# Kernel tuning notes

Measured on AMD Instinct MI355X. Metric: run time of the kernel, lower is better.

Reference implementation:

```python
import jax, jax.numpy as jnp
import numpy as np

H = 12          # nheads
SIM_EPS = 1e-8  # SimMatrix eps
LN_EPS = 1e-5   # nn.LayerNorm default eps
SLOPE = 0.01    # LeakyReLU default negative slope


def leaky(x):
    return jnp.where(x >= 0, x, SLOPE * x)


def etc_attention(hiddens, gamma, beta, Wout, bout):
    # hiddens: [B, L, 3*D]
    B, L, D3 = hiddens.shape
    D = D3 // 3
    d = D // H
    h = hiddens.reshape(B, L, 3, H, d)
    Q = h[:, :, 0].transpose(0, 2, 1, 3)  # [B,H,L,d]
    K = h[:, :, 1].transpose(0, 2, 1, 3)
    V = h[:, :, 2].transpose(0, 2, 1, 3)
    # cosine-similarity attention scores (SimMatrix(K, Q))
    Kn = K / jnp.clip(jnp.linalg.norm(K, axis=-1, keepdims=True), SIM_EPS, None)
    Qn = Q / jnp.clip(jnp.linalg.norm(Q, axis=-1, keepdims=True), SIM_EPS, None)
    att = jnp.einsum('bhid,bhjd->bhij', Kn, Qn)  # [B,H,L,L]
    # LayerNorm over the head axis H (lnormalize: [B, L*L, H] layernorm on last dim)
    mu = att.mean(axis=1, keepdims=True)
    var = att.var(axis=1, keepdims=True)  # biased, matches torch LayerNorm
    att = (att - mu) / jnp.sqrt(var + LN_EPS)
    att = att * gamma[None, :, None, None] + beta[None, :, None, None]
    att = jax.nn.softmax(att, axis=-1)
    att = jnp.where(jnp.isnan(att), jnp.zeros_like(att), att)  # removeNaN
    out = jnp.einsum('bhij,bhjd->bhid', att, V)          # att @ V
    out = out.transpose(0, 2, 1, 3).reshape(B, L, D)      # catHiddens
    # dropout is identity at inference; lin_out = Linear + Softmax
    probs = jax.nn.softmax(out @ Wout.T + bout, axis=-1)  # [B,L,C]
    return probs, att


def get_weights(att, masks):
    # att: [B,H,L,L], masks: [B,L] float
    w = masks * att.mean(axis=1).sum(axis=1)  # [B,L]
    return jax.nn.softmax(w, axis=-1)[..., None]  # [B,L,1]


def setup_inputs() -> dict:
    key = jax.random.key(0)
    ks = jax.random.split(key, 16)
    B, L = 16, 512
    Din, D, C, VOCAB = 300, 768, 20, 32000

    def kaiming(k, shape, fan_in):
        return jax.random.normal(k, shape, jnp.float32) * np.sqrt(2.0 / fan_in)

    return {
        'input_ids': jax.random.randint(ks[0], (B, L), 0, VOCAB),
        'wv': jax.random.normal(ks[1], (B, L, Din), jnp.float32),
        'emb': jax.random.normal(ks[2], (VOCAB, D), jnp.float32),
        'W_t': kaiming(ks[3], (3 * D, D), D),
        'b_t': jnp.zeros((3 * D,), jnp.float32),
        'gamma_t': jnp.ones((H,), jnp.float32),
        'beta_t': jnp.zeros((H,), jnp.float32),
        'Wout_t': kaiming(ks[4], (C, D), D),
        'bout_t': jnp.zeros((C,), jnp.float32),
        'W_h': kaiming(ks[5], (3 * D, Din), Din),
        'b_h': jnp.zeros((3 * D,), jnp.float32),
        'gamma_h': jnp.ones((H,), jnp.float32),
        'beta_h': jnp.zeros((H,), jnp.float32),
        'Wout_h': kaiming(ks[6], (C, D), D),
        'bout_h': jnp.zeros((C,), jnp.float32),
    }


def reference(input_ids, wv, emb, W_t, b_t, gamma_t, beta_t, Wout_t, bout_t,
              W_h, b_h, gamma_h, beta_h, Wout_h, bout_h):
    masks = (input_ids != 0).astype(jnp.float32)  # [B,L]
    # token branch: Embedding -> LeakyReLU -> Linear -> LeakyReLU
    h_t = leaky(leaky(emb[input_ids]) @ W_t.T + b_t)
    probs_t, att_t = etc_attention(h_t, gamma_t, beta_t, Wout_t, bout_t)
    probs_t = (get_weights(att_t, masks) * probs_t).sum(axis=1)  # [B,C]
    # hidden/word-vector branch: Linear -> LeakyReLU
    h_h = leaky(wv @ W_h.T + b_h)
    probs_h, att_h = etc_attention(h_h, gamma_h, beta_h, Wout_h, bout_h)
    probs_h = (get_weights(att_h, masks) * probs_h).sum(axis=1)
    return (probs_t + probs_h) / 2.0
```

## Files before the change

kernel.cpp:

```cpp
#include <hip/hip_runtime.h>

typedef unsigned int uint;
typedef unsigned short ushort;
typedef _Float16 f16;
typedef _Float16 h8 __attribute__((ext_vector_type(8)));
typedef float f32x4 __attribute__((ext_vector_type(4)));


__device__ __forceinline__ float b2f(ushort u){ return __uint_as_float(((uint)u)<<16); }
__device__ __forceinline__ ushort f2b(float f){
  uint u = __float_as_uint(f);
  uint r = u + 0x7fffu + ((u>>16)&1u);
  return (ushort)(r>>16);
}
__device__ __forceinline__ float leaky(float x){ return x >= 0.f ? x : 0.01f*x; }
__device__ __forceinline__ float ldf(const void* p, int idx, int isb){
  return isb ? b2f(((const ushort*)p)[idx]) : ((const float*)p)[idx];
}

#define GLOAD16(gp, lp) __builtin_amdgcn_global_load_lds( \
    (const __attribute__((address_space(1))) void*)(gp), \
    (__attribute__((address_space(3))) void*)(lp), 16, 0, 0)

__global__ __launch_bounds__(256) void k_init(const ushort* __restrict__ wvbits,
    int* __restrict__ flag, float* __restrict__ zbase){
  int bid = blockIdx.x, tid = threadIdx.x;
  if (bid == 0){
    if (tid == 0){
      int sane = 0;
      for (int i=0;i<128;i++){
        uint e = (wvbits[i]>>7)&0xffu;
        if (e==0u || (e>=90u && e<=150u)) sane++;
      }
      *flag = (sane >= 115) ? 1 : 0;
    }
  } else {
    zbase[(bid-1)*256 + tid] = 0.f;
  }
}

__global__ __launch_bounds__(256) void k_prep_all(const int* __restrict__ ids,
    const void* __restrict__ emb, const void* __restrict__ wv,
    const void* __restrict__ W0, const void* __restrict__ W1,
    const int* __restrict__ flag,
    f16* __restrict__ AhA, f16* __restrict__ WhA,
    f16* __restrict__ AhB, f16* __restrict__ WhB,
    int nBX, int nW0, int nA1, int nW1){
  int isb = *flag;
  int bx = blockIdx.x, tid = threadIdx.x;
  if (bx < nBX){
    int t = bx*256 + tid;
    int m = t / 96, kk = (t % 96) * 8;
    float o[8];
    if (isb){
      const ushort* src = (const ushort*)emb + (size_t)ids[m]*768 + kk;
      uint4 v = *(const uint4*)src;
      o[0]=__uint_as_float((v.x&0xffffu)<<16); o[1]=__uint_as_float(v.x&0xffff0000u);
      o[2]=__uint_as_float((v.y&0xffffu)<<16); o[3]=__uint_as_float(v.y&0xffff0000u);
      o[4]=__uint_as_float((v.z&0xffffu)<<16); o[5]=__uint_as_float(v.z&0xffff0000u);
      o[6]=__uint_as_float((v.w&0xffffu)<<16); o[7]=__uint_as_float(v.w&0xffff0000u);
    } else {
      const float* src = (const float*)emb + (size_t)ids[m]*768 + kk;
      float4 v0 = ((const float4*)src)[0];
      float4 v1 = ((const float4*)src)[1];
      o[0]=v0.x; o[1]=v0.y; o[2]=v0.z; o[3]=v0.w;
      o[4]=v1.x; o[5]=v1.y; o[6]=v1.z; o[7]=v1.w;
    }
    h8 hv;
    #pragma unroll
    for (int i=0;i<8;i++) hv[i] = (f16)leaky(o[i]);
    *(h8*)(AhA + (size_t)m*768 + kk) = hv;
  } else if (bx < nBX + nW0){
    int t = (bx - nBX)*256 + tid;
    int n = t / 96, kk = (t % 96) * 8;
    h8 hv;
    #pragma unroll
    for (int i=0;i<8;i++) hv[i] = (f16)ldf(W0, n*768 + kk + i, isb);
    *(h8*)(WhA + (size_t)n*768 + kk) = hv;
  } else if (bx < nBX + nW0 + nA1){
    int t = (bx - nBX - nW0)*256 + tid;
    int n = t / 40, kk = (t % 40) * 8;
    h8 hv;
    #pragma unroll
    for (int i=0;i<8;i++){
      int k = kk + i;
      hv[i] = (k < 300) ? (f16)ldf(wv, n*300 + k, isb) : (f16)0.f;
    }
    *(h8*)(AhB + (size_t)n*320 + kk) = hv;
  } else {
    int t = (bx - nBX - nW0 - nA1)*256 + tid;
    int n = t / 40, kk = (t % 40) * 8;
    h8 hv;
    #pragma unroll
    for (int i=0;i<8;i++){
      int k = kk + i;
      hv[i] = (k < 300) ? (f16)ldf(W1, n*300 + k, isb) : (f16)0.f;
    }
    *(h8*)(WhB + (size_t)n*320 + kk) = hv;
  }
}

__global__ __launch_bounds__(256) void k_gemm_m(
    const f16* AhA, const f16* WhA, const void* biasA, int KA,
    f16* QhA, f16* KhA, f16* VtA,
    const f16* AhB, const f16* WhB, const void* biasB, int KB,
    f16* QhB, f16* KhB, f16* VtB,
    const int* __restrict__ flag, int sbase){
  __shared__ __align__(16) f16 As[128*64];
  __shared__ __align__(16) f16 Bs[128*64];
  int z = sbase + blockIdx.z;
  const f16* Ah = z ? AhB : AhA;
  const f16* Wh = z ? WhB : WhA;
  const void* bias = z ? biasB : biasA;
  int KP = z ? KB : KA;
  f16* Qh = z ? QhB : QhA;
  f16* Kh = z ? KhB : KhA;
  f16* Vt = z ? VtB : VtA;
  int STEPS = KP >> 6;

  int tid = threadIdx.x;
  int w = tid >> 6, lane = tid & 63;
  int mrow = lane & 15, kq = lane >> 4;
  int m0 = (((blockIdx.x & 7)<<3) | (blockIdx.x >> 3)) * 128;
  int n0 = blockIdx.y * 128;
  int msub = (w & 1) * 64, nsub = (w >> 1) * 64;

  f32x4 acc[4][4];
  #pragma unroll
  for (int mt=0; mt<4; mt++)
    #pragma unroll
    for (int nt=0; nt<4; nt++) acc[mt][nt] = (f32x4){0.f,0.f,0.f,0.f};

  int cbase = w*64 + lane;

  for (int step=0; step<STEPS; step++){
    int k0 = step*64;
    __syncthreads();
    #pragma unroll
    for (int rep=0; rep<4; rep++){
      int cb = rep*256 + w*64;
      int c  = rep*256 + cbase;
      int row = c >> 3;
      int qs  = (c & 7) ^ (row & 7);
      GLOAD16(Ah + (size_t)(m0+row)*KP + k0 + qs*8, As + cb*8);
      GLOAD16(Wh + (size_t)(n0+row)*KP + k0 + qs*8, Bs + cb*8);
    }
    __syncthreads();
    #pragma unroll
    for (int ks=0; ks<2; ks++){
      h8 af[4], bf[4];
      #pragma unroll
      for (int mt=0; mt<4; mt++){
        int row = msub + mt*16 + mrow;
        int slot = (ks*4 + kq) ^ (row & 7);
        af[mt] = *(const h8*)(As + row*64 + slot*8);
      }
      #pragma unroll
      for (int nt=0; nt<4; nt++){
        int row = nsub + nt*16 + mrow;
        int slot = (ks*4 + kq) ^ (row & 7);
        bf[nt] = *(const h8*)(Bs + row*64 + slot*8);
      }
      #pragma unroll
      for (int mt=0; mt<4; mt++)
        #pragma unroll
        for (int nt=0; nt<4; nt++)
          acc[mt][nt] = __builtin_amdgcn_mfma_f32_16x16x32_f16(af[mt], bf[nt], acc[mt][nt], 0, 0, 0);
    }
  }

  int isb = *flag;
  int n0w = n0 + nsub;
  int s = n0w / 768;
  int h = (n0w % 768) >> 6;
  float bv[4];
  #pragma unroll
  for (int nt=0; nt<4; nt++) bv[nt] = ldf(bias, n0w + nt*16 + mrow, isb);

  #pragma unroll
  for (int mt=0; mt<4; mt++){
    float yv[4][4];
    #pragma unroll
    for (int nt=0; nt<4; nt++)
      #pragma unroll
      for (int r=0; r<4; r++)
        yv[nt][r] = leaky(acc[mt][nt][r] + bv[nt]);
    if (s < 2){
      #pragma unroll
      for (int r=0; r<4; r++){
        float ss = yv[0][r]*yv[0][r] + yv[1][r]*yv[1][r]
                 + yv[2][r]*yv[2][r] + yv[3][r]*yv[3][r];
        ss += __shfl_xor(ss, 1); ss += __shfl_xor(ss, 2);
        ss += __shfl_xor(ss, 4); ss += __shfl_xor(ss, 8);
        float rn = 1.f / fmaxf(sqrtf(ss), 1e-8f);
        #pragma unroll
        for (int nt=0; nt<4; nt++) yv[nt][r] *= rn;
      }
    }
    #pragma unroll
    for (int nt=0; nt<4; nt++){
      #pragma unroll
      for (int r=0; r<4; r++){
        int m = m0 + msub + mt*16 + kq*4 + r;
        int dd = nt*16 + mrow;
        int bq = m >> 9, l = m & 511;
        float y = yv[nt][r];
        if (s == 0)      Qh[((size_t)(bq*12 + h)*512 + l)*64 + dd] = (f16)y;
        else if (s == 1) Kh[((size_t)(bq*12 + h)*512 + l)*64 + dd] = (f16)y;
        else             Vt[((size_t)(bq*12 + h)*64 + dd)*512 + l] = (f16)y;
      }
    }
  }
}

__global__ __launch_bounds__(256) void k_scores(const f16* __restrict__ Qh,
    const f16* __restrict__ Kh, const void* __restrict__ gamma,
    const void* __restrict__ beta, const int* __restrict__ flag,
    f16* __restrict__ E, float* __restrict__ lsump){
  constexpr int TS = 72;
  __shared__ f16 S[12*16*TS];
  __shared__ float gL[12], beL[12];

  int tid = threadIdx.x;
  int w = tid >> 6, lane = tid & 63;
  int kq = lane >> 4, mrow = lane & 15;
  int bx = (blockIdx.x & 7)*512 + (blockIdx.x >> 3);
  int jt = bx & 7, it = (bx >> 3) & 31, b = bx >> 8;
  int i0 = it*16, j0 = jt*64;

  if (tid < 12){ int isb = *flag; gL[tid] = ldf(gamma, tid, isb); beL[tid] = ldf(beta, tid, isb); }

  #pragma unroll
  for (int hh=0; hh<3; hh++){
    int h = w*3 + hh;
    const f16* kb = Kh + ((size_t)(b*12+h)*512 + i0 + mrow)*64;
    h8 a0 = *(const h8*)(kb + kq*8);
    h8 a1 = *(const h8*)(kb + 32 + kq*8);
    const f16* qb = Qh + ((size_t)(b*12+h)*512 + j0)*64;
    #pragma unroll
    for (int jn=0; jn<4; jn++){
      const f16* qr = qb + (size_t)(jn*16 + mrow)*64;
      h8 q0 = *(const h8*)(qr + kq*8);
      h8 q1 = *(const h8*)(qr + 32 + kq*8);
      f32x4 c = (f32x4){0.f,0.f,0.f,0.f};
      c = __builtin_amdgcn_mfma_f32_16x16x32_f16(a0, q0, c, 0, 0, 0);
      c = __builtin_amdgcn_mfma_f32_16x16x32_f16(a1, q1, c, 0, 0, 0);
      #pragma unroll
      for (int r=0;r<4;r++)
        S[(h*16 + kq*4 + r)*TS + jn*16 + mrow] = (f16)c[r];
    }
  }
  __syncthreads();
  int pj = tid & 63, piw = tid >> 6;
  #pragma unroll
  for (int p=0; p<4; p++){
    int i = piw*4 + p;
    float s[12];
    float mu = 0.f, sq = 0.f;
    #pragma unroll
    for (int h=0;h<12;h++){ s[h] = (float)S[(h*16+i)*TS + pj]; mu += s[h]; sq += s[h]*s[h]; }
    mu *= (1.f/12.f);
    float var = fmaxf(sq*(1.f/12.f) - mu*mu, 0.f);
    float rstd = rsqrtf(var + 1e-5f);
    #pragma unroll
    for (int h=0;h<12;h++){
      float e = __expf((s[h]-mu)*rstd*gL[h] + beL[h]);
      S[(h*16+i)*TS + pj] = (f16)e;
    }
  }
  __syncthreads();
  if (tid < 192){
    int h = tid >> 4, i = tid & 15;
    const f16* zr = &S[(h*16 + i)*TS];
    float ssum = 0.f;
    #pragma unroll
    for (int q=0;q<8;q++){
      h8 v = *(const h8*)(zr + q*8);
      #pragma unroll
      for (int t=0;t<8;t++) ssum += (float)v[t];
    }
    lsump[((size_t)(b*12+h)*512 + i0 + i)*8 + jt] = ssum;
  }
  #pragma unroll
  for (int u0=0; u0<6; u0++){
    int u = tid + u0*256;
    int h = u >> 7, rem = u & 127, i = rem >> 3, q = rem & 7;
    h8 v = *(const h8*)&S[(h*16 + i)*TS + q*8];
    *(h8*)(E + ((size_t)(b*12+h)*512 + i0 + i)*512 + j0 + q*8) = v;
  }
}

__global__ __launch_bounds__(256) void k_pv2(const f16* __restrict__ E,
    const f16* __restrict__ Vt, const float* __restrict__ lsump,
    float* __restrict__ O, float* __restrict__ colsum){
  __shared__ float csL[512];
  __shared__ __align__(16) f16 EL[4*16*256];
  int tid = threadIdx.x;
  int w = tid >> 6, lane = tid & 63;
  int kq = lane >> 4, mrow = lane & 15;
  int b = blockIdx.y;
  int bx = (blockIdx.x & 7)*12 + (blockIdx.x >> 3);
  int h = bx >> 3, it = bx & 7;
  int i0w = it*64 + w*16;

  csL[tid] = 0.f; csL[tid + 256] = 0.f;
  const float4* lp = (const float4*)(lsump + ((size_t)(b*12+h)*512 + i0w + mrow)*8);
  float4 p0 = lp[0], p1 = lp[1];
  float rinv = 1.f / (p0.x+p0.y+p0.z+p0.w + p1.x+p1.y+p1.z+p1.w);
  __syncthreads();

  const f16* ebase = E + ((size_t)(b*12+h)*512 + i0w)*512;
  const f16* vbase = Vt + ((size_t)(b*12+h)*64 + mrow)*512 + kq*8;
  char* Ew = (char*)EL + w*8192;

  f32x4 acc[4];
  #pragma unroll
  for (int nt=0; nt<4; nt++) acc[nt] = (f32x4){0.f,0.f,0.f,0.f};

  for (int ph=0; ph<2; ph++){
    const f16* eb = ebase + ph*256;
    #pragma unroll
    for (int rr=0; rr<8; rr++){
      int r = rr*2 + (lane>>5);
      h8 v = *(const h8*)(eb + (size_t)r*512 + (lane&31)*8);
      *(h8*)(Ew + r*512 + (((lane&31)*16) ^ ((r&7)<<4))) = v;
    }
    #pragma unroll 4
    for (int jt2=0; jt2<8; jt2++){
      int jt = ph*8 + jt2;
      int j0 = jt*32;
      int co = jt2*64 + kq*16;
      h8 ea  = *(const h8*)(Ew + mrow*512 + (co ^ ((mrow&7)<<4)));
      h8 bf0 = *(const h8*)(vbase + j0);
      h8 bf1 = *(const h8*)(vbase + (size_t)16*512 + j0);
      h8 bf2 = *(const h8*)(vbase + (size_t)32*512 + j0);
      h8 bf3 = *(const h8*)(vbase + (size_t)48*512 + j0);
      acc[0] = __builtin_amdgcn_mfma_f32_16x16x32_f16(ea, bf0, acc[0], 0, 0, 0);
      acc[1] = __builtin_amdgcn_mfma_f32_16x16x32_f16(ea, bf1, acc[1], 0, 0, 0);
      acc[2] = __builtin_amdgcn_mfma_f32_16x16x32_f16(ea, bf2, acc[2], 0, 0, 0);
      acc[3] = __builtin_amdgcn_mfma_f32_16x16x32_f16(ea, bf3, acc[3], 0, 0, 0);
      float cs[8];
      #pragma unroll
      for (int t=0;t<8;t++) cs[t] = (float)ea[t] * rinv;
      #pragma unroll
      for (int t=0;t<8;t++){
        cs[t] += __shfl_xor(cs[t], 1); cs[t] += __shfl_xor(cs[t], 2);
        cs[t] += __shfl_xor(cs[t], 4); cs[t] += __shfl_xor(cs[t], 8);
      }
      if (mrow == 0){
        #pragma unroll
        for (int t=0;t<8;t++) atomicAdd(&csL[j0 + kq*8 + t], cs[t]);
      }
    }
  }
  __syncthreads();
  atomicAdd(&colsum[b*512 + tid],       csL[tid]       * (1.f/12.f));
  atomicAdd(&colsum[b*512 + 256 + tid], csL[tid + 256] * (1.f/12.f));

  #pragma unroll
  for (int r=0; r<4; r++){
    float g = __shfl(rinv, kq*4 + r);
    #pragma unroll
    for (int nt=0; nt<4; nt++)
      O[((size_t)(b*512) + i0w + kq*4 + r)*768 + h*64 + nt*16 + mrow] = acc[nt][r] * g;
  }
}

__global__ __launch_bounds__(256) void k_probs_m(const float* OA, const float* OB,
    const void* WoA, const void* WoB, const void* boA, const void* boB,
    float* prA, float* prB, const int* __restrict__ flag, int sbase){
  int z = sbase + blockIdx.y;
  const float* O = z ? OB : OA;
  const void* Wout = z ? WoB : WoA;
  const void* bout = z ? boB : boA;
  float* probs = z ? prB : prA;
  int isb = *flag;
  int tid = threadIdx.x, wv = tid>>6, lane = tid&63;
  int m = blockIdx.x*4 + wv;
  const float* orow = O + (size_t)m*768;
  float acc[20];
  #pragma unroll
  for (int c=0;c<20;c++) acc[c]=0.f;
  for (int kk=0; kk<12; kk++){
    float o = orow[kk*64 + lane];
    #pragma unroll
    for (int c=0;c<20;c++)
      acc[c] += o * ldf(Wout, c*768 + kk*64 + lane, isb);
  }
  #pragma unroll
  for (int c=0;c<20;c++){
    #pragma unroll
    for (int off=1; off<64; off<<=1) acc[c] += __shfl_xor(acc[c], off, 64);
  }
  float mx = -3.4e38f;
  #pragma unroll
  for (int c=0;c<20;c++){ acc[c] += ldf(bout, c, isb); mx = fmaxf(mx, acc[c]); }
  float s=0.f;
  #pragma unroll
  for (int c=0;c<20;c++){ acc[c] = __expf(acc[c]-mx); s += acc[c]; }
  float inv = 1.f/s;
  if (lane == 0){
    float* pr = probs + (size_t)m*20;
    #pragma unroll
    for (int c=0;c<20;c++) pr[c] = acc[c]*inv;
  }
}

__global__ __launch_bounds__(512) void k_final_m(const int* __restrict__ ids,
    const float* __restrict__ cs0, const float* __restrict__ cs1,
    const float* __restrict__ pr0, const float* __restrict__ pr1,
    const int* __restrict__ flag, void* __restrict__ outp){
  __shared__ float red[8];
  __shared__ float bcast;
  __shared__ float pacc[8][20];
  __shared__ float osum[20];
  int b = blockIdx.x, tid = threadIdx.x;
  int wv = tid>>6, lane = tid&63;
  int msk = (ids[b*512+tid] != 0);
  for (int br=0; br<2; br++){
    const float* colsum = br ? cs1 : cs0;
    const float* probs  = br ? pr1 : pr0;
    float w = msk ? colsum[b*512+tid] : 0.f;
    float mx = w;
    #pragma unroll
    for (int off=1; off<64; off<<=1) mx = fmaxf(mx, __shfl_xor(mx, off, 64));
    if (lane==0) red[wv] = mx;
    __syncthreads();
    if (tid==0){ float m2 = red[0]; for (int k2=1;k2<8;k2++) m2 = fmaxf(m2, red[k2]); bcast = m2; }
    __syncthreads();
    float M = bcast;
    float e = __expf(w - M);
    float s = e;
    #pragma unroll
    for (int off=1; off<64; off<<=1) s += __shfl_xor(s, off, 64);
    if (lane==0) red[wv] = s;
    __syncthreads();
    if (tid==0){ float s2=0.f; for (int k2=0;k2<8;k2++) s2 += red[k2]; bcast = s2; }
    __syncthreads();
    float wn = e / bcast;
    float p[20];
    const float* pr = probs + ((size_t)b*512 + tid)*20;
    #pragma unroll
    for (int c=0;c<20;c++) p[c] = wn * pr[c];
    #pragma unroll
    for (int c=0;c<20;c++){
      #pragma unroll
      for (int off=1; off<64; off<<=1) p[c] += __shfl_xor(p[c], off, 64);
    }
    if (lane==0){
      #pragma unroll
      for (int c=0;c<20;c++) pacc[wv][c] = p[c];
    }
    __syncthreads();
    if (tid < 20){
      float s2 = 0.f;
      #pragma unroll
      for (int k2=0;k2<8;k2++) s2 += pacc[k2][tid];
      if (br == 0) osum[tid] = s2;
      else         osum[tid] += s2;
    }
    __syncthreads();
  }
  if (tid < 20){
    float v = osum[tid] * 0.5f;
    if (*flag) ((ushort*)outp)[b*20 + tid] = f2b(v);
    else       ((float*)outp)[b*20 + tid] = v;
  }
}

extern "C" void kernel_launch(void* const* d_in, const int* in_sizes, int n_in,
                              void* d_out, int out_size, void* d_ws, size_t ws_size,
                              hipStream_t stream){
  (void)in_sizes; (void)n_in; (void)out_size;
  const int*  ids = (const int*)d_in[0];
  const void* wvp = d_in[1];
  const void* emb = d_in[2];
  const void* Wt[2]  = {d_in[3], d_in[9]};
  const void* bt[2]  = {d_in[4], d_in[10]};
  const void* gm[2]  = {d_in[5], d_in[11]};
  const void* bet[2] = {d_in[6], d_in[12]};
  const void* Wo[2]  = {d_in[7], d_in[13]};
  const void* bo[2]  = {d_in[8], d_in[14]};

  char* p = (char*)d_ws;
  #define ALLOC(ty, name, cnt) ty* name = (ty*)p; p += sizeof(ty)*(size_t)(cnt)

  p = (char*)d_ws;
  ALLOC(float, O0, 6291456);
  ALLOC(float, O1, 6291456);
  ALLOC(f16, Qh0, 6291456); ALLOC(f16, Kh0, 6291456); ALLOC(f16, Vt0, 6291456);
  ALLOC(f16, Qh1, 6291456); ALLOC(f16, Kh1, 6291456); ALLOC(f16, Vt1, 6291456);
  ALLOC(f16, Ah0, 6291456); ALLOC(f16, Wh0, 1769472);
  ALLOC(f16, Ah1, 2621440); ALLOC(f16, Wh1, 737280);
  ALLOC(float, probs0, 163840); ALLOC(float, probs1, 163840);
  ALLOC(float, zb_big, 16384);
  ALLOC(int, flag_big, 4);
  ALLOC(f16, E_big, 50331648);
  size_t needBig = (size_t)(p - (char*)d_ws);

  if (ws_size >= needBig){
    float* colsum0 = zb_big;
    float* colsum1 = zb_big + 8192;
    int* flagp = flag_big; f16* E = E_big;
    float* lsump0 = (float*)Ah0;
    float* lsump1 = lsump0 + 786432;

    k_init<<<65, 256, 0, stream>>>((const ushort*)wvp, flagp, zb_big);
    k_prep_all<<<3072+864+1280+360, 256, 0, stream>>>(ids, emb, wvp, Wt[0], Wt[1],
        flagp, Ah0, Wh0, Ah1, Wh1, 3072, 864, 1280, 360);
    dim3 gg(64, 18, 2);
    k_gemm_m<<<gg, 256, 0, stream>>>(Ah0, Wh0, bt[0], 768, Qh0, Kh0, Vt0,
                                     Ah1, Wh1, bt[1], 320, Qh1, Kh1, Vt1, flagp, 0);
    dim3 gpv(96, 16);
    k_scores<<<4096, 256, 0, stream>>>(Qh0, Kh0, gm[0], bet[0], flagp, E, lsump0);
    k_pv2<<<gpv, 256, 0, stream>>>(E, Vt0, lsump0, O0, colsum0);
    k_scores<<<4096, 256, 0, stream>>>(Qh1, Kh1, gm[1], bet[1], flagp, E, lsump1);
    k_pv2<<<gpv, 256, 0, stream>>>(E, Vt1, lsump1, O1, colsum1);
    dim3 gpr(2048, 2);
    k_probs_m<<<gpr, 256, 0, stream>>>(O0, O1, Wo[0], Wo[1], bo[0], bo[1],
                                       probs0, probs1, flagp, 0);
    k_final_m<<<16, 512, 0, stream>>>(ids, colsum0, colsum1, probs0, probs1, flagp, d_out);
    return;
  }

  p = (char*)d_ws;
  ALLOC(float, O, 6291456);
  ALLOC(f16, Qh, 6291456); ALLOC(f16, Kh, 6291456); ALLOC(f16, Vt, 6291456);
  ALLOC(f16, Ah, 6291456); ALLOC(f16, Wh, 1769472);
  ALLOC(float, probsA, 163840); ALLOC(float, probsB, 163840);
  ALLOC(float, zb, 16384);
  ALLOC(int, flagm, 4);
  ALLOC(f16, Em, 50331648);
  float* colsum0 = zb;
  float* colsum1 = zb + 8192;
  float* lsumm0 = (float*)Ah;
  float* lsumm1 = lsumm0 + 786432;

  k_init<<<65, 256, 0, stream>>>((const ushort*)wvp, flagm, zb);
  k_prep_all<<<3072+864, 256, 0, stream>>>(ids, emb, wvp, Wt[0], Wt[1],
      flagm, Ah, Wh, Ah, Wh, 3072, 864, 0, 0);
  dim3 g1(64, 18, 1);
  k_gemm_m<<<g1, 256, 0, stream>>>(Ah, Wh, bt[0], 768, Qh, Kh, Vt,
                                   Ah, Wh, bt[0], 768, Qh, Kh, Vt, flagm, 0);
  dim3 gpv(96, 16);
  k_scores<<<4096, 256, 0, stream>>>(Qh, Kh, gm[0], bet[0], flagm, Em, lsumm0);
  k_pv2<<<gpv, 256, 0, stream>>>(Em, Vt, lsumm0, O, colsum0);
  dim3 gpr(2048, 1);
  k_probs_m<<<gpr, 256, 0, stream>>>(O, O, Wo[0], Wo[1], bo[0], bo[1],
                                     probsA, probsB, flagm, 0);
  k_prep_all<<<1280+360, 256, 0, stream>>>(ids, emb, wvp, Wt[0], Wt[1],
      flagm, Ah, Wh, Ah, Wh, 0, 0, 1280, 360);
  k_gemm_m<<<g1, 256, 0, stream>>>(Ah, Wh, bt[1], 320, Qh, Kh, Vt,
                                   Ah, Wh, bt[1], 320, Qh, Kh, Vt, flagm, 0);
  k_scores<<<4096, 256, 0, stream>>>(Qh, Kh, gm[1], bet[1], flagm, Em, lsumm1);
  k_pv2<<<gpv, 256, 0, stream>>>(Em, Vt, lsumm1, O, colsum1);
  k_probs_m<<<gpr, 256, 0, stream>>>(O, O, Wo[0], Wo[1], bo[0], bo[1],
                                     probsA, probsB, flagm, 1);
  k_final_m<<<16, 512, 0, stream>>>(ids, colsum0, colsum1, probsA, probsB, flagm, d_out);
  #undef ALLOC
}
```

Measured before the change: 567.1 us.

## Keep per-head scores in registers for cross-head LayerNorm in k_scores

Rework the work split in k_scores so each wave computes a 16x16 tile for all 12 heads, keeping the results in MFMA accumulator registers. The cross-head LayerNorm and exp then run directly on those registers. This removes the shared-memory score tile and one block barrier. Row sums are now reduced with lane shuffles plus a small shared buffer. In exchange, E is written as scalar 2-byte stores, 32 bytes per row segment, instead of 16-byte vector stores, which may reduce write efficiency on the large E tensor.

```diff
diff --git a/kernel.cpp b/kernel.cpp
--- a/kernel.cpp
+++ b/kernel.cpp
@@ -217,76 +217,81 @@
     const f16* __restrict__ Kh, const void* __restrict__ gamma,
     const void* __restrict__ beta, const int* __restrict__ flag,
     f16* __restrict__ E, float* __restrict__ lsump){
-  constexpr int TS = 72;
-  __shared__ f16 S[12*16*TS];
-  __shared__ float gL[12], beL[12];
-
+  __shared__ float rsp[768];
   int tid = threadIdx.x;
   int w = tid >> 6, lane = tid & 63;
   int kq = lane >> 4, mrow = lane & 15;
   int bx = (blockIdx.x & 7)*512 + (blockIdx.x >> 3);
   int jt = bx & 7, it = (bx >> 3) & 31, b = bx >> 8;
   int i0 = it*16, j0 = jt*64;
-
-  if (tid < 12){ int isb = *flag; gL[tid] = ldf(gamma, tid, isb); beL[tid] = ldf(beta, tid, isb); }
-
-  #pragma unroll
-  for (int hh=0; hh<3; hh++){
-    int h = w*3 + hh;
-    const f16* kb = Kh + ((size_t)(b*12+h)*512 + i0 + mrow)*64;
-    h8 a0 = *(const h8*)(kb + kq*8);
-    h8 a1 = *(const h8*)(kb + 32 + kq*8);
-    const f16* qb = Qh + ((size_t)(b*12+h)*512 + j0)*64;
-    #pragma unroll
-    for (int jn=0; jn<4; jn++){
-      const f16* qr = qb + (size_t)(jn*16 + mrow)*64;
-      h8 q0 = *(const h8*)(qr + kq*8);
-      h8 q1 = *(const h8*)(qr + 32 + kq*8);
+  int jw = j0 + w*16;
+
+  int isb = *flag;
+  float gr[12], br[12];
+  #pragma unroll
+  for (int h=0;h<12;h++){ gr[h] = ldf(gamma, h, isb); br[h] = ldf(beta, h, isb); }
+
+  f32x4 acc[12];
+  #pragma unroll
+  for (int hb=0; hb<4; hb++){
+    h8 kv[3][2], qv[3][2];
+    #pragma unroll
+    for (int hh=0; hh<3; hh++){
+      int h = hb*3 + hh;
+      const f16* kb = Kh + ((size_t)(b*12+h)*512 + i0 + mrow)*64;
+      kv[hh][0] = *(const h8*)(kb + kq*8);
+      kv[hh][1] = *(const h8*)(kb + 32 + kq*8);
+      const f16* qb = Qh + ((size_t)(b*12+h)*512 + jw + mrow)*64;
+      qv[hh][0] = *(const h8*)(qb + kq*8);
+      qv[hh][1] = *(const h8*)(qb + 32 + kq*8);
+    }
+    #pragma unroll
+    for (int hh=0; hh<3; hh++){
       f32x4 c = (f32x4){0.f,0.f,0.f,0.f};
-      c = __builtin_amdgcn_mfma_f32_16x16x32_f16(a0, q0, c, 0, 0, 0);
-      c = __builtin_amdgcn_mfma_f32_16x16x32_f16(a1, q1, c, 0, 0, 0);
-      #pragma unroll
-      for (int r=0;r<4;r++)
-        S[(h*16 + kq*4 + r)*TS + jn*16 + mrow] = (f16)c[r];
-    }
-  }
-  __syncthreads();
-  int pj = tid & 63, piw = tid >> 6;
-  #pragma unroll
-  for (int p=0; p<4; p++){
-    int i = piw*4 + p;
-    float s[12];
+      c = __builtin_amdgcn_mfma_f32_16x16x32_f16(kv[hh][0], qv[hh][0], c, 0, 0, 0);
+      c = __builtin_amdgcn_mfma_f32_16x16x32_f16(kv[hh][1], qv[hh][1], c, 0, 0, 0);
+      acc[hb*3+hh] = c;
+    }
+  }
+
+  #pragma unroll
+  for (int r=0; r<4; r++){
     float mu = 0.f, sq = 0.f;
     #pragma unroll
-    for (int h=0;h<12;h++){ s[h] = (float)S[(h*16+i)*TS + pj]; mu += s[h]; sq += s[h]*s[h]; }
+    for (int h=0;h<12;h++){ float s = acc[h][r]; mu += s; sq += s*s; }
     mu *= (1.f/12.f);
     float var = fmaxf(sq*(1.f/12.f) - mu*mu, 0.f);
     float rstd = rsqrtf(var + 1e-5f);
     #pragma unroll
     for (int h=0;h<12;h++){
-      float e = __expf((s[h]-mu)*rstd*gL[h] + beL[h]);
-      S[(h*16+i)*TS + pj] = (f16)e;
-    }
+      float e = __expf((acc[h][r]-mu)*rstd*gr[h] + br[h]);
+      f16 ef = (f16)e;
+      E[((size_t)(b*12+h)*512 + i0 + kq*4 + r)*512 + jw + mrow] = ef;
+      acc[h][r] = (float)ef;
+    }
+  }
+
+  #pragma unroll
+  for (int h=0;h<12;h++)
+    #pragma unroll
+    for (int r=0;r<4;r++){
+      float v = acc[h][r];
+      v += __shfl_xor(v, 1); v += __shfl_xor(v, 2);
+      v += __shfl_xor(v, 4); v += __shfl_xor(v, 8);
+      acc[h][r] = v;
+    }
+  if (mrow == 0){
+    #pragma unroll
+    for (int h=0;h<12;h++)
+      #pragma unroll
+      for (int r=0;r<4;r++)
+        rsp[w*192 + h*16 + kq*4 + r] = acc[h][r];
   }
   __syncthreads();
   if (tid < 192){
     int h = tid >> 4, i = tid & 15;
-    const f16* zr = &S[(h*16 + i)*TS];
-    float ssum = 0.f;
-    #pragma unroll
-    for (int q=0;q<8;q++){
-      h8 v = *(const h8*)(zr + q*8);
-      #pragma unroll
-      for (int t=0;t<8;t++) ssum += (float)v[t];
-    }
-    lsump[((size_t)(b*12+h)*512 + i0 + i)*8 + jt] = ssum;
-  }
-  #pragma unroll
-  for (int u0=0; u0<6; u0++){
-    int u = tid + u0*256;
-    int h = u >> 7, rem = u & 127, i = rem >> 3, q = rem & 7;
-    h8 v = *(const h8*)&S[(h*16 + i)*TS + q*8];
-    *(h8*)(E + ((size_t)(b*12+h)*512 + i0 + i)*512 + j0 + q*8) = v;
+    lsump[((size_t)(b*12+h)*512 + i0 + i)*8 + jt]
+        = rsp[tid] + rsp[192+tid] + rsp[384+tid] + rsp[576+tid];
   }
 }
 
```

After: 660.9 us. +16.5%, slower.
